# Optimization experiments

Hardware: AMD Instinct MI355X
Metric: run time of the kernel (lower is better)

The kernel has to match this reference:

```python
import jax, jax.numpy as jnp
import numpy as np

N_GRAPHS = 8
NODES_PER_G = 1024
EDGES_PER_G = 2048
N = N_GRAPHS * NODES_PER_G          # 8192 nodes
E = N_GRAPHS * EDGES_PER_G          # 16384 edges
IN_DIM, EDGE_DIM, HID, OUT_DIM, T = 10, 9, 64, 3, 5
EPS = 1e-6


def _lin(key, fan_in, fan_out):
    kw, kb = jax.random.split(key)
    s = 1.0 / np.sqrt(fan_in)
    return (jax.random.uniform(kw, (fan_in, fan_out), jnp.float32, -s, s),
            jax.random.uniform(kb, (fan_out,), jnp.float32, -s, s))


def setup_inputs() -> dict:
    key = jax.random.key(0)
    ks = jax.random.split(key, 32)
    x = jax.random.normal(ks[0], (N, IN_DIM), jnp.float32)
    edge_attr = jax.random.normal(ks[1], (E, EDGE_DIM), jnp.float32)
    # edges stay within their own graph (block structure)
    src_l = jax.random.randint(ks[2], (E,), 0, NODES_PER_G)
    dst_l = jax.random.randint(ks[3], (E,), 0, NODES_PER_G)
    off = jnp.repeat(jnp.arange(N_GRAPHS, dtype=jnp.int64) * NODES_PER_G, EDGES_PER_G)
    edge_index = jnp.stack([src_l.astype(jnp.int64) + off, dst_l.astype(jnp.int64) + off])
    batch = jnp.repeat(jnp.arange(N_GRAPHS, dtype=jnp.int64), NODES_PER_G)

    lift_w1, lift_b1 = _lin(ks[4], IN_DIM, HID)
    lift_w2, lift_b2 = _lin(ks[5], HID, HID)
    proj_w1, proj_b1 = _lin(ks[6], HID, HID)
    proj_w2, proj_b2 = _lin(ks[7], HID, OUT_DIM)

    def stackp(fn, base):
        ws, bs = zip(*[fn(ks[base + t]) for t in range(T)])
        return jnp.stack(ws), jnp.stack(bs)

    root_w, root_b = stackp(lambda k: _lin(k, HID, HID), 8)
    k_w1, k_b1 = stackp(lambda k: _lin(k, EDGE_DIM, HID), 13)
    k_w2, k_b2 = stackp(lambda k: _lin(k, HID, HID), 18)
    k_w3, k_b3 = stackp(lambda k: _lin(k, HID, HID * HID), 23)

    return dict(x=x, edge_attr=edge_attr,
                lift_w1=lift_w1, lift_b1=lift_b1, lift_w2=lift_w2, lift_b2=lift_b2,
                root_w=root_w, root_b=root_b,
                k_w1=k_w1, k_b1=k_b1, k_w2=k_w2, k_b2=k_b2, k_w3=k_w3, k_b3=k_b3,
                proj_w1=proj_w1, proj_b1=proj_b1, proj_w2=proj_w2, proj_b2=proj_b2,
                edge_index=edge_index, batch=batch)


def reference(x, edge_attr, lift_w1, lift_b1, lift_w2, lift_b2,
              root_w, root_b, k_w1, k_b1, k_w2, k_b2, k_w3, k_b3,
              proj_w1, proj_b1, proj_w2, proj_b2, edge_index, batch):
    src, dst = edge_index[0], edge_index[1]

    # --- per-graph edge_attr standardization (scatter mean/std over each graph's edges) ---
    eb = batch[src]                                           # graph id per edge [E]
    ones_e = jnp.ones((E,), jnp.float32)
    cnt = jax.ops.segment_sum(ones_e, eb, num_segments=N_GRAPHS)          # [G]
    mean = jax.ops.segment_sum(edge_attr, eb, num_segments=N_GRAPHS) / cnt[:, None]
    msq = jax.ops.segment_sum(edge_attr * edge_attr, eb, num_segments=N_GRAPHS) / cnt[:, None]
    std = jnp.sqrt(jnp.clip(msq - mean * mean, 0.0))
    ea = (edge_attr - mean[eb]) / (std[eb] + EPS)             # [E, edge_dim]

    # --- lift MLP ---
    v = jax.nn.relu(x @ lift_w1 + lift_b1) @ lift_w2 + lift_b2  # [N, HID]

    # --- T kernel layers: v' = relu(W_root v + mean_{j->i} K(e_ij) v_j) ---
    deg = jnp.clip(jax.ops.segment_sum(ones_e, dst, num_segments=N), 1.0)  # [N]
    for t in range(T):
        h = jax.nn.relu(ea @ k_w1[t] + k_b1[t])
        h = jax.nn.relu(h @ k_w2[t] + k_b2[t])
        ker = (h @ k_w3[t] + k_b3[t]).reshape(E, HID, HID)    # per-edge 64x64 kernel
        msg = jnp.einsum('eij,ej->ei', ker, v[src])           # [E, HID]
        aggr = jax.ops.segment_sum(msg, dst, num_segments=N) / deg[:, None]
        v = jax.nn.relu(v @ root_w[t] + root_b[t] + aggr)
        # dropout (p=0.1) is identity in eval mode

    # --- project MLP ---
    return jax.nn.relu(v @ proj_w1 + proj_b1) @ proj_w2 + proj_b2  # [N, OUT_DIM]
```

## Files before the change

### kernel.cpp

```cpp
#include <hip/hip_runtime.h>

#define N_GRAPHS    8
#define EDGES_PER_G 2048
#define NN          8192
#define EE          16384
#define IN_DIM      10
#define EDGE_DIM    9
#define HID         64
#define OUT_DIM     3
#define TT          5
#define EPSN        1e-6f

typedef float f32x4 __attribute__((ext_vector_type(4)));
typedef short bf16x8s __attribute__((ext_vector_type(8)));

union BF8 { __bf16 h[8]; bf16x8s v; };

__device__ inline void edgemlp_body_T(int e0, int tid,
    const float* __restrict__ ear, const float* __restrict__ meanb,
    const float* __restrict__ invstd,
    const float* __restrict__ w1, const float* __restrict__ b1,
    const float* __restrict__ w2, const float* __restrict__ b2,
    float (*sh)[HID], float (*st)[HID], float* __restrict__ h2T) {
  int g = tid >> 6, lane = tid & 63;
  int e = e0 + g;
  int gg = e >> 11;
  const float* er = ear + (size_t)e * EDGE_DIM;
  const float* mb = meanb + gg * EDGE_DIM;
  const float* is = invstd + gg * EDGE_DIM;
  float xn[EDGE_DIM];
#pragma unroll
  for (int d = 0; d < EDGE_DIM; ++d) xn[d] = (er[d] - mb[d]) * is[d];
  float a = b1[lane];
#pragma unroll
  for (int d = 0; d < EDGE_DIM; ++d) a += xn[d] * w1[d * HID + lane];
  sh[g][lane] = fmaxf(a, 0.f);
  __syncthreads();
  float o = b2[lane];
#pragma unroll
  for (int h = 0; h < HID; ++h) o += sh[g][h] * w2[h * HID + lane];
  st[g][lane] = fmaxf(o, 0.f);
  __syncthreads();
  int c = tid >> 2, eo = tid & 3;
  h2T[(size_t)c * EE + e0 + eo] = st[eo][c];
}

__global__ __launch_bounds__(256) void k_stats(
    const float* __restrict__ ear, float* __restrict__ meanb,
    float* __restrict__ invstd, float* __restrict__ degf) {
  __shared__ float sw[4][2 * EDGE_DIM];
  int b = blockIdx.x;
  int g = threadIdx.x >> 6, lane = threadIdx.x & 63;
  if (b < N_GRAPHS) {
    int gg = b;
    float ls[EDGE_DIM], lq[EDGE_DIM];
#pragma unroll
    for (int d = 0; d < EDGE_DIM; ++d) { ls[d] = 0.f; lq[d] = 0.f; }
    for (int e = threadIdx.x; e < EDGES_PER_G; e += blockDim.x) {
      const float* row = ear + (size_t)(gg * EDGES_PER_G + e) * EDGE_DIM;
#pragma unroll
      for (int d = 0; d < EDGE_DIM; ++d) { float xv = row[d]; ls[d] += xv; lq[d] += xv * xv; }
    }
#pragma unroll
    for (int d = 0; d < EDGE_DIM; ++d) {
#pragma unroll
      for (int off = 32; off > 0; off >>= 1) {
        ls[d] += __shfl_down(ls[d], off);
        lq[d] += __shfl_down(lq[d], off);
      }
    }
    if (lane == 0) {
#pragma unroll
      for (int d = 0; d < EDGE_DIM; ++d) {
        sw[g][d] = ls[d];
        sw[g][EDGE_DIM + d] = lq[d];
      }
    }
    __syncthreads();
    if (threadIdx.x < EDGE_DIM) {
      int d = threadIdx.x;
      float s0 = sw[0][d] + sw[1][d] + sw[2][d] + sw[3][d];
      float q0 = sw[0][EDGE_DIM + d] + sw[1][EDGE_DIM + d] +
                 sw[2][EDGE_DIM + d] + sw[3][EDGE_DIM + d];
      float m  = s0 * (1.0f / EDGES_PER_G);
      float mq = q0 * (1.0f / EDGES_PER_G);
      float var = fmaxf(mq - m * m, 0.f);
      meanb[gg * EDGE_DIM + d]  = m;
      invstd[gg * EDGE_DIM + d] = 1.f / (sqrtf(var) + EPSN);
    }
  } else {
    int idx = (b - N_GRAPHS) * 256 + threadIdx.x;
    ((float4*)degf)[idx] = make_float4(0.f, 0.f, 0.f, 0.f);
  }
}

__global__ __launch_bounds__(256) void k_pre(
    const float* __restrict__ x,
    const float* __restrict__ lw1, const float* __restrict__ lb1,
    const float* __restrict__ lw2, const float* __restrict__ lb2,
    float* __restrict__ v,
    const float* __restrict__ kw3, const float* __restrict__ kb3,
    unsigned short* __restrict__ Bbf,
    const int* __restrict__ dst, float* __restrict__ degf,
    const float* __restrict__ ear, const float* __restrict__ meanb,
    const float* __restrict__ invstd, float* __restrict__ aggr,
    const float* __restrict__ w1, const float* __restrict__ b1,
    const float* __restrict__ w2, const float* __restrict__ b2,
    float* __restrict__ h2T0) {
  __shared__ float sh[4][HID];
  __shared__ float st[4][HID];
  int b = blockIdx.x;
  int g = threadIdx.x >> 6, lane = threadIdx.x & 63;
  if (b < EE / 4) {
    edgemlp_body_T(b * 4, threadIdx.x, ear, meanb, invstd, w1, b1, w2, b2,
                   sh, st, h2T0);
  } else if (b < EE / 4 + NN / 4) {
    int n = (b - EE / 4) * 4 + g;
    const float* xr = x + n * IN_DIM;
    float a = lb1[lane];
#pragma unroll
    for (int d = 0; d < IN_DIM; ++d) a += xr[d] * lw1[d * HID + lane];
    sh[g][lane] = fmaxf(a, 0.f);
    __syncthreads();
    float o = lb2[lane];
#pragma unroll
    for (int h = 0; h < HID; ++h) o += sh[g][h] * lw2[h * HID + lane];
    v[n * HID + lane] = o;
  } else if (b < EE / 4 + NN / 4 + 1024) {
    const int total = TT * 65 * 4096;
    for (int i = (b - (EE / 4 + NN / 4)) * 256 + (int)threadIdx.x; i < total;
         i += 1024 * 256) {
      int xx   = i & 4095;
      int call = i >> 12;
      int t = call / 65;
      int c = call - t * 65;
      int sn = xx >> 9;
      int s  = sn >> 2, nt = sn & 3;
      int l9 = xx & 511;
      int ln = l9 >> 3, jj = l9 & 7;
      int nn15 = ln & 15, qq = ln >> 4;
      int x_in = (nt * 16 + nn15) * 64 + s * 32 + qq * 8 + jj;
      float val = (c < 64) ? kw3[(size_t)(t * 64 + c) * 4096 + x_in]
                           : kb3[(size_t)t * 4096 + x_in];
      union { __bf16 h; unsigned short s16; } u;
      u.h = (__bf16)val;
      Bbf[i] = u.s16;
    }
  } else if (b < EE / 4 + NN / 4 + 1024 + EE / 256) {
    int e = (b - (EE / 4 + NN / 4 + 1024)) * 256 + threadIdx.x;
    atomicAdd(&degf[dst[e]], 1.f);
  } else {
    int idx = (b - (EE / 4 + NN / 4 + 1024 + EE / 256)) * 256 + threadIdx.x;
    ((float4*)aggr)[idx] = make_float4(0.f, 0.f, 0.f, 0.f);
  }
}

__global__ __launch_bounds__(256) void k_msg(const float* __restrict__ v,
    const float* __restrict__ h2T_r, const unsigned short* __restrict__ Bt,
    const int* __restrict__ src, const int* __restrict__ dst,
    float* __restrict__ aggr, int nEm,
    const float* __restrict__ ear, const float* __restrict__ meanb,
    const float* __restrict__ invstd,
    const float* __restrict__ w1, const float* __restrict__ b1,
    const float* __restrict__ w2, const float* __restrict__ b2,
    float* __restrict__ h2T_w) {
  __shared__ float red[4][32][68];
  int b = blockIdx.x;
  if (b < 512) {
    int w    = threadIdx.x >> 6;
    int lane = threadIdx.x & 63;
    int n15  = lane & 15;
    int q    = lane >> 4;
    int ebase = b * 32;

    bf16x8s ubf[2][2];
#pragma unroll
    for (int mt = 0; mt < 2; ++mt) {
      int e = ebase + mt * 16 + n15;
      const float4* vr = (const float4*)(v + (size_t)src[e] * HID);
      int f0 = q * 2;
#pragma unroll
      for (int s = 0; s < 2; ++s) {
        float4 pa = vr[s * 8 + f0], pb = vr[s * 8 + f0 + 1];
        BF8 u;
        u.h[0] = (__bf16)pa.x; u.h[1] = (__bf16)pa.y;
        u.h[2] = (__bf16)pa.z; u.h[3] = (__bf16)pa.w;
        u.h[4] = (__bf16)pb.x; u.h[5] = (__bf16)pb.y;
        u.h[6] = (__bf16)pb.z; u.h[7] = (__bf16)pb.w;
        ubf[mt][s] = u.v;
      }
    }

    f32x4 acc[2][4];
#pragma unroll
    for (int mt = 0; mt < 2; ++mt)
#pragma unroll
      for (int nt = 0; nt < 4; ++nt) acc[mt][nt] = (f32x4)0.0f;

    int c0 = w * 16;
    const unsigned short* Bp = Bt + (size_t)c0 * 4096 + lane * 8;
    const float* hq = h2T_r + (size_t)c0 * EE + ebase + q * 4;

#pragma unroll 4
    for (int cc = 0; cc < 16; ++cc) {
      const unsigned short* Bc = Bp + (size_t)cc * 4096;
      bf16x8s bfr[2][4];
#pragma unroll
      for (int s = 0; s < 2; ++s)
#pragma unroll
        for (int nt = 0; nt < 4; ++nt)
          bfr[s][nt] = *(const bf16x8s*)(Bc + (s * 4 + nt) * 512);
      float4 h4[2];
      h4[0] = *(const float4*)(hq + (size_t)cc * EE);
      h4[1] = *(const float4*)(hq + (size_t)cc * EE + 16);
      f32x4 tmp[2][4];
#pragma unroll
      for (int mt = 0; mt < 2; ++mt)
#pragma unroll
        for (int nt = 0; nt < 4; ++nt) {
          f32x4 t0 = __builtin_amdgcn_mfma_f32_16x16x32_bf16(
              ubf[mt][0], bfr[0][nt], (f32x4)0.0f, 0, 0, 0);
          tmp[mt][nt] = __builtin_amdgcn_mfma_f32_16x16x32_bf16(
              ubf[mt][1], bfr[1][nt], t0, 0, 0, 0);
        }
#pragma unroll
      for (int mt = 0; mt < 2; ++mt) {
        float4 hh = h4[mt];
#pragma unroll
        for (int nt = 0; nt < 4; ++nt) {
          acc[mt][nt][0] += hh.x * tmp[mt][nt][0];
          acc[mt][nt][1] += hh.y * tmp[mt][nt][1];
          acc[mt][nt][2] += hh.z * tmp[mt][nt][2];
          acc[mt][nt][3] += hh.w * tmp[mt][nt][3];
        }
      }
    }

    if (w == 3) {
      const unsigned short* Bc = Bt + (size_t)64 * 4096 + lane * 8;
      bf16x8s bfr[2][4];
#pragma unroll
      for (int s = 0; s < 2; ++s)
#pragma unroll
        for (int nt = 0; nt < 4; ++nt)
          bfr[s][nt] = *(const bf16x8s*)(Bc + (s * 4 + nt) * 512);
#pragma unroll
      for (int s = 0; s < 2; ++s)
#pragma unroll
        for (int mt = 0; mt < 2; ++mt)
#pragma unroll
          for (int nt = 0; nt < 4; ++nt)
            acc[mt][nt] = __builtin_amdgcn_mfma_f32_16x16x32_bf16(
                ubf[mt][s], bfr[s][nt], acc[mt][nt], 0, 0, 0);
    }

#pragma unroll
    for (int mt = 0; mt < 2; ++mt)
#pragma unroll
      for (int nt = 0; nt < 4; ++nt)
#pragma unroll
        for (int r = 0; r < 4; ++r)
          red[w][mt * 16 + q * 4 + r][nt * 16 + n15] = acc[mt][nt][r];
    __syncthreads();

    for (int i = threadIdx.x; i < 32 * HID; i += 256) {
      int e = i >> 6, c = i & 63;
      float s = red[0][e][c] + red[1][e][c] + red[2][e][c] + red[3][e][c];
      atomicAdd(aggr + (size_t)dst[ebase + e] * HID + c, s);
    }
  } else if (b < 512 + nEm) {
    float (*sh)[HID] = (float (*)[HID])&red[0][0][0];
    float (*st)[HID] = (float (*)[HID])(&red[0][0][0] + 4 * HID);
    edgemlp_body_T((b - 512) * 4, threadIdx.x, ear, meanb, invstd,
                   w1, b1, w2, b2, sh, st, h2T_w);
  }
}

__global__ __launch_bounds__(256) void k_upd(
    float* __restrict__ v, const float* __restrict__ rw, const float* __restrict__ rb,
    float* __restrict__ aggr, const float* __restrict__ degf) {
  __shared__ float sh[4][HID];
  int g = threadIdx.x >> 6, lane = threadIdx.x & 63;
  int n = blockIdx.x * 4 + g;
  int idx = n * HID + lane;
  sh[g][lane] = v[idx];
  __syncthreads();
  float inv = 1.f / fmaxf(degf[n], 1.f);
  float o = rb[lane] + aggr[idx] * inv;
  aggr[idx] = 0.f;
#pragma unroll
  for (int h = 0; h < HID; ++h) o += sh[g][h] * rw[h * HID + lane];
  v[idx] = fmaxf(o, 0.f);
}

__global__ __launch_bounds__(256) void k_upd_proj(
    const float* __restrict__ v, const float* __restrict__ rw,
    const float* __restrict__ rb,
    const float* __restrict__ aggr, const float* __restrict__ degf,
    const float* __restrict__ pw1, const float* __restrict__ pb1,
    const float* __restrict__ pw2, const float* __restrict__ pb2,
    float* __restrict__ out) {
  __shared__ float sh[4][HID];
  int g = threadIdx.x >> 6, lane = threadIdx.x & 63;
  int n = blockIdx.x * 4 + g;
  int idx = n * HID + lane;
  sh[g][lane] = v[idx];
  __syncthreads();
  float inv = 1.f / fmaxf(degf[n], 1.f);
  float o = rb[lane] + aggr[idx] * inv;
#pragma unroll
  for (int h = 0; h < HID; ++h) o += sh[g][h] * rw[h * HID + lane];
  float vn = fmaxf(o, 0.f);
  __syncthreads();
  sh[g][lane] = vn;
  __syncthreads();
  float a = pb1[lane];
#pragma unroll
  for (int h = 0; h < HID; ++h) a += sh[g][h] * pw1[h * HID + lane];
  float h1 = fmaxf(a, 0.f);
  __syncthreads();
  sh[g][lane] = h1;
  __syncthreads();
  if (lane < OUT_DIM) {
    float oo = pb2[lane];
#pragma unroll
    for (int h = 0; h < HID; ++h) oo += sh[g][h] * pw2[h * OUT_DIM + lane];
    out[n * OUT_DIM + lane] = oo;
  }
}

extern "C" void kernel_launch(void* const* d_in, const int* in_sizes, int n_in,
                              void* d_out, int out_size, void* d_ws, size_t ws_size,
                              hipStream_t stream) {
  const float* x        = (const float*)d_in[0];
  const float* ear      = (const float*)d_in[1];
  const float* lift_w1  = (const float*)d_in[2];
  const float* lift_b1  = (const float*)d_in[3];
  const float* lift_w2  = (const float*)d_in[4];
  const float* lift_b2  = (const float*)d_in[5];
  const float* root_w   = (const float*)d_in[6];
  const float* root_b   = (const float*)d_in[7];
  const float* kw1      = (const float*)d_in[8];
  const float* kb1      = (const float*)d_in[9];
  const float* kw2      = (const float*)d_in[10];
  const float* kb2      = (const float*)d_in[11];
  const float* kw3      = (const float*)d_in[12];
  const float* kb3      = (const float*)d_in[13];
  const float* pw1      = (const float*)d_in[14];
  const float* pb1      = (const float*)d_in[15];
  const float* pw2      = (const float*)d_in[16];
  const float* pb2      = (const float*)d_in[17];
  const int* edge_index = (const int*)d_in[18];
  const int* src = edge_index;
  const int* dst = edge_index + EE;
  float* out = (float*)d_out;

  float* ws     = (float*)d_ws;
  float* aggr   = ws;
  float* degf   = aggr + NN * HID;
  float* h2Ta   = degf + NN;
  float* h2Tb   = h2Ta + (size_t)HID * EE;
  float* vbuf   = h2Tb + (size_t)HID * EE;
  float* meanb  = vbuf + NN * HID;
  float* invstd = meanb + 72;
  unsigned short* Bbf = (unsigned short*)(invstd + 72);

  k_stats<<<2 * N_GRAPHS, 256, 0, stream>>>(ear, meanb, invstd, degf);

  const int PRE_BLOCKS = EE / 4 + NN / 4 + 1024 + EE / 256 + NN * HID / 1024;
  k_pre<<<PRE_BLOCKS, 256, 0, stream>>>(
      x, lift_w1, lift_b1, lift_w2, lift_b2, vbuf, kw3, kb3, Bbf,
      dst, degf, ear, meanb, invstd, aggr,
      kw1, kb1, kw2, kb2, h2Ta);

  for (int t = 0; t < TT; ++t) {
    const float* hr = (t & 1) ? h2Tb : h2Ta;
    float*       hw = (t & 1) ? h2Ta : h2Tb;
    int nEm = (t < TT - 1) ? EE / 4 : 0;
    int tt  = (t < TT - 1) ? t + 1 : t;
    k_msg<<<512 + nEm, 256, 0, stream>>>(
        vbuf, hr, Bbf + (size_t)t * 65 * 4096, src, dst, aggr, nEm,
        ear, meanb, invstd,
        kw1 + (size_t)tt * EDGE_DIM * HID, kb1 + (size_t)tt * HID,
        kw2 + (size_t)tt * HID * HID, kb2 + (size_t)tt * HID, hw);
    if (t < TT - 1) {
      k_upd<<<NN / 4, 256, 0, stream>>>(
          vbuf, root_w + (size_t)t * HID * HID, root_b + (size_t)t * HID,
          aggr, degf);
    } else {
      k_upd_proj<<<NN / 4, 256, 0, stream>>>(
          vbuf, root_w + (size_t)t * HID * HID, root_b + (size_t)t * HID,
          aggr, degf, pw1, pb1, pw2, pb2, out);
    }
  }
}
```

Baseline: 366.5 us.

## Process more edges per block in edge MLP and message kernels

The edge MLP now handles 16 edges per block (4 per wavefront), so each w1/w2 weight load is reused across four edges. The message kernel doubles its edge tile from 32 to 64 per block, which halves the number of reads of the bf16 kernel-weight slices. Its cross-wave reduction now uses shared-memory atomics into one zeroed buffer instead of four separate partial buffers. The trade-offs are more register pressure (acc grows to 16 f32x4 per lane), fewer blocks in the message phase (256), and contention on the LDS atomics.

```diff
diff --git a/kernel.cpp b/kernel.cpp
--- a/kernel.cpp
+++ b/kernel.cpp
@@ -16,33 +16,54 @@
 
 union BF8 { __bf16 h[8]; bf16x8s v; };
 
-__device__ inline void edgemlp_body_T(int e0, int tid,
+__device__ inline void edgemlp16(int e0, int tid,
     const float* __restrict__ ear, const float* __restrict__ meanb,
     const float* __restrict__ invstd,
     const float* __restrict__ w1, const float* __restrict__ b1,
     const float* __restrict__ w2, const float* __restrict__ b2,
-    float (*sh)[HID], float (*st)[HID], float* __restrict__ h2T) {
+    float* smem, float* __restrict__ h2T) {
+  float (*sh)[68] = (float (*)[68])smem;
+  float (*st)[68] = (float (*)[68])(smem + 16 * 68);
   int g = tid >> 6, lane = tid & 63;
-  int e = e0 + g;
-  int gg = e >> 11;
-  const float* er = ear + (size_t)e * EDGE_DIM;
+  int eb = e0 + g * 4;
+  int gg = e0 >> 11;
   const float* mb = meanb + gg * EDGE_DIM;
   const float* is = invstd + gg * EDGE_DIM;
-  float xn[EDGE_DIM];
-#pragma unroll
-  for (int d = 0; d < EDGE_DIM; ++d) xn[d] = (er[d] - mb[d]) * is[d];
-  float a = b1[lane];
-#pragma unroll
-  for (int d = 0; d < EDGE_DIM; ++d) a += xn[d] * w1[d * HID + lane];
-  sh[g][lane] = fmaxf(a, 0.f);
-  __syncthreads();
-  float o = b2[lane];
-#pragma unroll
-  for (int h = 0; h < HID; ++h) o += sh[g][h] * w2[h * HID + lane];
-  st[g][lane] = fmaxf(o, 0.f);
-  __syncthreads();
-  int c = tid >> 2, eo = tid & 3;
-  h2T[(size_t)c * EE + e0 + eo] = st[eo][c];
+  float xn[4][EDGE_DIM];
+#pragma unroll
+  for (int k = 0; k < 4; ++k) {
+    const float* er = ear + (size_t)(eb + k) * EDGE_DIM;
+#pragma unroll
+    for (int d = 0; d < EDGE_DIM; ++d) xn[k][d] = (er[d] - mb[d]) * is[d];
+  }
+  float a0 = b1[lane], a1 = a0, a2 = a0, a3 = a0;
+#pragma unroll
+  for (int d = 0; d < EDGE_DIM; ++d) {
+    float w = w1[d * HID + lane];
+    a0 += xn[0][d] * w; a1 += xn[1][d] * w;
+    a2 += xn[2][d] * w; a3 += xn[3][d] * w;
+  }
+  sh[g * 4 + 0][lane] = fmaxf(a0, 0.f);
+  sh[g * 4 + 1][lane] = fmaxf(a1, 0.f);
+  sh[g * 4 + 2][lane] = fmaxf(a2, 0.f);
+  sh[g * 4 + 3][lane] = fmaxf(a3, 0.f);
+  __syncthreads();
+  float o0 = b2[lane], o1 = o0, o2 = o0, o3 = o0;
+#pragma unroll
+  for (int h = 0; h < HID; ++h) {
+    float w = w2[h * HID + lane];
+    o0 += sh[g * 4 + 0][h] * w; o1 += sh[g * 4 + 1][h] * w;
+    o2 += sh[g * 4 + 2][h] * w; o3 += sh[g * 4 + 3][h] * w;
+  }
+  st[g * 4 + 0][lane] = fmaxf(o0, 0.f);
+  st[g * 4 + 1][lane] = fmaxf(o1, 0.f);
+  st[g * 4 + 2][lane] = fmaxf(o2, 0.f);
+  st[g * 4 + 3][lane] = fmaxf(o3, 0.f);
+  __syncthreads();
+  for (int i = tid; i < HID * 16; i += 256) {
+    int c = i >> 4, eo = i & 15;
+    h2T[(size_t)c * EE + e0 + eo] = st[eo][c];
+  }
 }
 
 __global__ __launch_bounds__(256) void k_stats(
@@ -94,6 +115,11 @@
   }
 }
 
+#define PRE_EM0   (EE / 16)
+#define PRE_LIFT  (NN / 4)
+#define PRE_BPREP 1024
+#define PRE_DEG   (EE / 256)
+#define PRE_ZAG   (NN * HID / 1024)
 __global__ __launch_bounds__(256) void k_pre(
     const float* __restrict__ x,
     const float* __restrict__ lw1, const float* __restrict__ lb1,
@@ -107,15 +133,15 @@
     const float* __restrict__ w1, const float* __restrict__ b1,
     const float* __restrict__ w2, const float* __restrict__ b2,
     float* __restrict__ h2T0) {
-  __shared__ float sh[4][HID];
-  __shared__ float st[4][HID];
+  __shared__ float smem[2 * 16 * 68];
   int b = blockIdx.x;
   int g = threadIdx.x >> 6, lane = threadIdx.x & 63;
-  if (b < EE / 4) {
-    edgemlp_body_T(b * 4, threadIdx.x, ear, meanb, invstd, w1, b1, w2, b2,
-                   sh, st, h2T0);
-  } else if (b < EE / 4 + NN / 4) {
-    int n = (b - EE / 4) * 4 + g;
+  if (b < PRE_EM0) {
+    edgemlp16(b * 16, threadIdx.x, ear, meanb, invstd, w1, b1, w2, b2,
+              smem, h2T0);
+  } else if (b < PRE_EM0 + PRE_LIFT) {
+    float (*sh)[HID] = (float (*)[HID])smem;
+    int n = (b - PRE_EM0) * 4 + g;
     const float* xr = x + n * IN_DIM;
     float a = lb1[lane];
 #pragma unroll
@@ -126,10 +152,10 @@
 #pragma unroll
     for (int h = 0; h < HID; ++h) o += sh[g][h] * lw2[h * HID + lane];
     v[n * HID + lane] = o;
-  } else if (b < EE / 4 + NN / 4 + 1024) {
+  } else if (b < PRE_EM0 + PRE_LIFT + PRE_BPREP) {
     const int total = TT * 65 * 4096;
-    for (int i = (b - (EE / 4 + NN / 4)) * 256 + (int)threadIdx.x; i < total;
-         i += 1024 * 256) {
+    for (int i = (b - (PRE_EM0 + PRE_LIFT)) * 256 + (int)threadIdx.x; i < total;
+         i += PRE_BPREP * 256) {
       int xx   = i & 4095;
       int call = i >> 12;
       int t = call / 65;
@@ -146,11 +172,11 @@
       u.h = (__bf16)val;
       Bbf[i] = u.s16;
     }
-  } else if (b < EE / 4 + NN / 4 + 1024 + EE / 256) {
-    int e = (b - (EE / 4 + NN / 4 + 1024)) * 256 + threadIdx.x;
+  } else if (b < PRE_EM0 + PRE_LIFT + PRE_BPREP + PRE_DEG) {
+    int e = (b - (PRE_EM0 + PRE_LIFT + PRE_BPREP)) * 256 + threadIdx.x;
     atomicAdd(&degf[dst[e]], 1.f);
   } else {
-    int idx = (b - (EE / 4 + NN / 4 + 1024 + EE / 256)) * 256 + threadIdx.x;
+    int idx = (b - (PRE_EM0 + PRE_LIFT + PRE_BPREP + PRE_DEG)) * 256 + threadIdx.x;
     ((float4*)aggr)[idx] = make_float4(0.f, 0.f, 0.f, 0.f);
   }
 }
@@ -164,18 +190,20 @@
     const float* __restrict__ w1, const float* __restrict__ b1,
     const float* __restrict__ w2, const float* __restrict__ b2,
     float* __restrict__ h2T_w) {
-  __shared__ float red[4][32][68];
+  __shared__ float smem[64 * 68];
   int b = blockIdx.x;
-  if (b < 512) {
+  if (b < 256) {
     int w    = threadIdx.x >> 6;
     int lane = threadIdx.x & 63;
     int n15  = lane & 15;
     int q    = lane >> 4;
-    int ebase = b * 32;
-
-    bf16x8s ubf[2][2];
-#pragma unroll
-    for (int mt = 0; mt < 2; ++mt) {
+    int ebase = b * 64;
+
+    for (int i = threadIdx.x; i < 64 * 68; i += 256) smem[i] = 0.f;
+
+    bf16x8s ubf[4][2];
+#pragma unroll
+    for (int mt = 0; mt < 4; ++mt) {
       int e = ebase + mt * 16 + n15;
       const float4* vr = (const float4*)(v + (size_t)src[e] * HID);
       int f0 = q * 2;
@@ -191,9 +219,9 @@
       }
     }
 
-    f32x4 acc[2][4];
-#pragma unroll
-    for (int mt = 0; mt < 2; ++mt)
+    f32x4 acc[4][4];
+#pragma unroll
+    for (int mt = 0; mt < 4; ++mt)
 #pragma unroll
       for (int nt = 0; nt < 4; ++nt) acc[mt][nt] = (f32x4)0.0f;
 
@@ -210,28 +238,27 @@
 #pragma unroll
         for (int nt = 0; nt < 4; ++nt)
           bfr[s][nt] = *(const bf16x8s*)(Bc + (s * 4 + nt) * 512);
-      float4 h4[2];
-      h4[0] = *(const float4*)(hq + (size_t)cc * EE);
-      h4[1] = *(const float4*)(hq + (size_t)cc * EE + 16);
-      f32x4 tmp[2][4];
-#pragma unroll
-      for (int mt = 0; mt < 2; ++mt)
+      float4 h4[4];
+#pragma unroll
+      for (int mt = 0; mt < 4; ++mt)
+        h4[mt] = *(const float4*)(hq + (size_t)cc * EE + mt * 16);
+#pragma unroll
+      for (int mt = 0; mt < 4; ++mt) {
+        f32x4 tmp[4];
 #pragma unroll
         for (int nt = 0; nt < 4; ++nt) {
           f32x4 t0 = __builtin_amdgcn_mfma_f32_16x16x32_bf16(
               ubf[mt][0], bfr[0][nt], (f32x4)0.0f, 0, 0, 0);
-          tmp[mt][nt] = __builtin_amdgcn_mfma_f32_16x16x32_bf16(
+          tmp[nt] = __builtin_amdgcn_mfma_f32_16x16x32_bf16(
               ubf[mt][1], bfr[1][nt], t0, 0, 0, 0);
         }
-#pragma unroll
-      for (int mt = 0; mt < 2; ++mt) {
         float4 hh = h4[mt];
 #pragma unroll
         for (int nt = 0; nt < 4; ++nt) {
-          acc[mt][nt][0] += hh.x * tmp[mt][nt][0];
-          acc[mt][nt][1] += hh.y * tmp[mt][nt][1];
-          acc[mt][nt][2] += hh.z * tmp[mt][nt][2];
-          acc[mt][nt][3] += hh.w * tmp[mt][nt][3];
+          acc[mt][nt][0] += hh.x * tmp[nt][0];
+          acc[mt][nt][1] += hh.y * tmp[nt][1];
+          acc[mt][nt][2] += hh.z * tmp[nt][2];
+          acc[mt][nt][3] += hh.w * tmp[nt][3];
         }
       }
     }
@@ -247,32 +274,31 @@
 #pragma unroll
       for (int s = 0; s < 2; ++s)
 #pragma unroll
-        for (int mt = 0; mt < 2; ++mt)
+        for (int mt = 0; mt < 4; ++mt)
 #pragma unroll
           for (int nt = 0; nt < 4; ++nt)
             acc[mt][nt] = __builtin_amdgcn_mfma_f32_16x16x32_bf16(
                 ubf[mt][s], bfr[s][nt], acc[mt][nt], 0, 0, 0);
     }
 
-#pragma unroll
-    for (int mt = 0; mt < 2; ++mt)
+    __syncthreads();
+#pragma unroll
+    for (int mt = 0; mt < 4; ++mt)
 #pragma unroll
       for (int nt = 0; nt < 4; ++nt)
 #pragma unroll
         for (int r = 0; r < 4; ++r)
-          red[w][mt * 16 + q * 4 + r][nt * 16 + n15] = acc[mt][nt][r];
+          atomicAdd(&smem[(mt * 16 + q * 4 + r) * 68 + nt * 16 + n15],
+                    acc[mt][nt][r]);
     __syncthreads();
 
-    for (int i = threadIdx.x; i < 32 * HID; i += 256) {
+    for (int i = threadIdx.x; i < 64 * HID; i += 256) {
       int e = i >> 6, c = i & 63;
-      float s = red[0][e][c] + red[1][e][c] + red[2][e][c] + red[3][e][c];
-      atomicAdd(aggr + (size_t)dst[ebase + e] * HID + c, s);
-    }
-  } else if (b < 512 + nEm) {
-    float (*sh)[HID] = (float (*)[HID])&red[0][0][0];
-    float (*st)[HID] = (float (*)[HID])(&red[0][0][0] + 4 * HID);
-    edgemlp_body_T((b - 512) * 4, threadIdx.x, ear, meanb, invstd,
-                   w1, b1, w2, b2, sh, st, h2T_w);
+      atomicAdd(aggr + (size_t)dst[ebase + e] * HID + c, smem[e * 68 + c]);
+    }
+  } else if (b < 256 + nEm) {
+    edgemlp16((b - 256) * 16, threadIdx.x, ear, meanb, invstd,
+              w1, b1, w2, b2, smem, h2T_w);
   }
 }
 
@@ -367,7 +393,7 @@
 
   k_stats<<<2 * N_GRAPHS, 256, 0, stream>>>(ear, meanb, invstd, degf);
 
-  const int PRE_BLOCKS = EE / 4 + NN / 4 + 1024 + EE / 256 + NN * HID / 1024;
+  const int PRE_BLOCKS = PRE_EM0 + PRE_LIFT + PRE_BPREP + PRE_DEG + PRE_ZAG;
   k_pre<<<PRE_BLOCKS, 256, 0, stream>>>(
       x, lift_w1, lift_b1, lift_w2, lift_b2, vbuf, kw3, kb3, Bbf,
       dst, degf, ear, meanb, invstd, aggr,
@@ -376,9 +402,9 @@
   for (int t = 0; t < TT; ++t) {
     const float* hr = (t & 1) ? h2Tb : h2Ta;
     float*       hw = (t & 1) ? h2Ta : h2Tb;
-    int nEm = (t < TT - 1) ? EE / 4 : 0;
+    int nEm = (t < TT - 1) ? EE / 16 : 0;
     int tt  = (t < TT - 1) ? t + 1 : t;
-    k_msg<<<512 + nEm, 256, 0, stream>>>(
+    k_msg<<<256 + nEm, 256, 0, stream>>>(
         vbuf, hr, Bbf + (size_t)t * 65 * 4096, src, dst, aggr, nEm,
         ear, meanb, invstd,
         kw1 + (size_t)tt * EDGE_DIM * HID, kb1 + (size_t)tt * HID,
```

Result: slower. 527.3 us (+43.9%).
